# Kernel tuning notes

Hardware: AMD Instinct MI355X
Metric: run time of the kernel (lower is better)

Reference implementation:

```python
import jax, jax.numpy as jnp
import numpy as np

V, E, H, L = 32000, 512, 1024, 2
B, S, T = 32, 64, 64


def setup_inputs() -> dict:
    key = jax.random.key(0)
    ks = jax.random.split(key, 16)
    sd = 0.05
    p = lambda k, shape: (jax.random.normal(k, shape, jnp.float32) * sd)
    z = lambda shape: jnp.zeros(shape, jnp.float32)
    return {
        "tgt_batch": jax.random.randint(ks[0], (B, S), 0, V),
        "enc_h": p(ks[1], (L, B, H)),
        "enc_c": p(ks[2], (L, B, H)),
        "enc_outputs": p(ks[3], (T, B, H)),
        "emb": p(ks[4], (V, E)),
        "W_ih0": p(ks[5], (4 * H, E + H)),
        "W_hh0": p(ks[6], (4 * H, H)),
        "b_ih0": z((4 * H,)),
        "b_hh0": z((4 * H,)),
        "W_ih1": p(ks[7], (4 * H, H)),
        "W_hh1": p(ks[8], (4 * H, H)),
        "b_ih1": z((4 * H,)),
        "b_hh1": z((4 * H,)),
        "Wa": p(ks[9], (H, 2 * H)),
        "ba": z((H,)),
        "va": p(ks[10], (H,)),
        "Wc": p(ks[11], (H, 2 * H)),
        "bc": z((H,)),
        "Wo": p(ks[12], (V, H)),
        "bo": z((V,)),
        "teacher_forcing": 1,
    }


def _lstm_cell(x, h, c, Wih, Whh, bih, bhh):
    # PyTorch gate order: i, f, g, o
    g = x @ Wih.T + bih + h @ Whh.T + bhh
    i, f, gg, o = jnp.split(g, 4, axis=1)
    c2 = jax.nn.sigmoid(f) * c + jax.nn.sigmoid(i) * jnp.tanh(gg)
    return jax.nn.sigmoid(o) * jnp.tanh(c2), c2


def reference(tgt_batch, enc_h, enc_c, enc_outputs, emb,
              W_ih0, W_hh0, b_ih0, b_hh0, W_ih1, W_hh1, b_ih1, b_hh1,
              Wa, ba, va, Wc, bc, Wo, bo, teacher_forcing):
    # teacher_forcing == 1 -> always feed the gold previous word (matches
    # the torch loop, whose sampling branch is never taken at tf=1.0).
    tgt = tgt_batch.T  # [S, B], seq-first

    def step(carry, x_t):
        h, c, attn_h = carry  # h,c: [L,B,H]; attn_h: [B,H]
        x = jnp.concatenate([emb[x_t], attn_h], axis=1)  # [B, E+H]
        h0, c0 = _lstm_cell(x, h[0], c[0], W_ih0, W_hh0, b_ih0, b_hh0)
        h1, c1 = _lstm_cell(h0, h[1], c[1], W_ih1, W_hh1, b_ih1, b_hh1)
        # additive ('concat') attention over encoder states, query = top h
        hid = jnp.broadcast_to(h1[None], enc_outputs.shape)  # [T,B,H]
        energy = jnp.tanh(jnp.concatenate([hid, enc_outputs], axis=-1) @ Wa.T + ba)
        scores = jnp.einsum('tbh,h->bt', energy, va)  # [B,T]
        weights = jax.nn.softmax(scores, axis=1)
        context = jnp.einsum('bt,tbh->bh', weights, enc_outputs)  # [B,H]
        attn_h2 = jnp.tanh(jnp.concatenate([h1, context], axis=1) @ Wc.T + bc)
        logp = jax.nn.log_softmax(attn_h2 @ Wo.T + bo, axis=1)  # [B,V]
        return (jnp.stack([h0, h1]), jnp.stack([c0, c1]), attn_h2), logp

    init = (enc_h, enc_c, jnp.zeros((tgt.shape[1], H), enc_h.dtype))
    _, dec_outputs = jax.lax.scan(step, init, tgt[:-1])  # [S-1, B, V]
    dec_output_words = jnp.argmax(dec_outputs, axis=-1).astype(jnp.int32)
    return dec_outputs, dec_output_words
```

## Files before the change

kernel.cpp:

```cpp
#include <hip/hip_runtime.h>
#include <math.h>

#define VOCAB 32000
#define EMBD  512
#define HID   1024
#define BATCH 32
#define SEQ   64
#define TENC  64
#define NSTEP 63
#define G4    4096

typedef __attribute__((ext_vector_type(8))) short short8;
typedef __attribute__((ext_vector_type(4))) float f32x4;
typedef __attribute__((ext_vector_type(4))) unsigned short us4;

__device__ __forceinline__ float4 ld4(const float* p) {
  return *reinterpret_cast<const float4*>(p);
}
__device__ __forceinline__ unsigned short f2bf(float x) {
  unsigned u = __float_as_uint(x);
  return (unsigned short)((u + 0x7fffu + ((u >> 16) & 1u)) >> 16);
}
__device__ __forceinline__ float bf2f(unsigned short h) {
  return __uint_as_float(((unsigned)h) << 16);
}

template<class FA, class FW>
__device__ __forceinline__ void g32x4(int team, int ttid, FA fa, FW fw, int KT,
                                      float* tiles, float* res) {
  float* At = tiles + team * 2176;
  float* Wt = At + 1088;
  const int lr = ttid >> 3, lc = (ttid & 7) << 2;
  const int tn = ttid & 15, tm = ttid >> 4;
  float a00=0.f, a01=0.f, a10=0.f, a11=0.f;
  float4 av = fa(lc);
  float4 wv = fw(lc);
  for (int k0 = 0; k0 < KT; k0 += 32) {
    float4 avn, wvn;
    if (k0 + 32 < KT) { avn = fa(k0 + 32 + lc); wvn = fw(k0 + 32 + lc); }
    __syncthreads();
    At[(lc+0)*34+lr]=av.x; At[(lc+1)*34+lr]=av.y; At[(lc+2)*34+lr]=av.z; At[(lc+3)*34+lr]=av.w;
    Wt[(lc+0)*34+lr]=wv.x; Wt[(lc+1)*34+lr]=wv.y; Wt[(lc+2)*34+lr]=wv.z; Wt[(lc+3)*34+lr]=wv.w;
    __syncthreads();
    #pragma unroll
    for (int kk = 0; kk < 32; ++kk) {
      const float2 a = *reinterpret_cast<const float2*>(&At[kk*34 + tm*2]);
      const float2 w = *reinterpret_cast<const float2*>(&Wt[kk*34 + tn*2]);
      a00 += a.x*w.x; a01 += a.x*w.y; a10 += a.y*w.x; a11 += a.y*w.y;
    }
    av = avn; wv = wvn;
  }
  float* r = res + team * 1056;
  r[(tm*2  )*33 + tn*2  ] = a00;
  r[(tm*2  )*33 + tn*2+1] = a01;
  r[(tm*2+1)*33 + tn*2  ] = a10;
  r[(tm*2+1)*33 + tn*2+1] = a11;
}

__device__ __forceinline__ void whh_block(const float* h, const float* W, float* C,
                                          int nt, int ldc, float* tiles, float* res) {
  const int tid = threadIdx.x, team = tid >> 8, ttid = tid & 255;
  const int lr = ttid >> 3;
  const int kb = team * 256;
  const float* Ap = h + lr*HID + kb;
  const float* Wp = W + (size_t)(nt*32 + lr)*HID + kb;
  g32x4(team, ttid, [=](int k){ return ld4(Ap + k); },
        [=](int k){ return ld4(Wp + k); }, 256, tiles, res);
  __syncthreads();
  const int b = tid >> 5, cc = tid & 31;
  const float v = res[b*33+cc] + res[1056 + b*33+cc]
                + res[2112 + b*33+cc] + res[3168 + b*33+cc];
  C[(size_t)b*ldc + nt*32 + cc] = v;
}

struct GC {
  const int* tgt; const float* emb;
  const float* A;
  const float* W;
  const float* gembt; const float* PgH; const float* bsum;
  float* h; float* c; int t;
};

template<int LAYER, int HOIST>
__device__ __forceinline__ void gcell_block(const GC& P, int nt, float* tiles, float* res) {
  const int tid = threadIdx.x, team = tid >> 8, ttid = tid & 255;
  const int lr = ttid >> 3;
  const int wrow = (lr >> 3)*1024 + nt*8 + (lr & 7);
  if (LAYER == 0) {
    if (HOIST) {
      const int kb = team * 256;
      const float* Ap = P.A + lr*HID + kb;
      const float* Wp = P.W + (size_t)wrow*(EMBD+HID) + EMBD + kb;
      g32x4(team, ttid, [=](int k){ return ld4(Ap + k); },
            [=](int k){ return ld4(Wp + k); }, 256, tiles, res);
    } else {
      const int kb = team * 384;
      const float* Wp = P.W + (size_t)wrow*(EMBD+HID) + kb;
      const int tok = P.tgt[lr*SEQ + P.t];
      const float* Ep = P.emb + (size_t)tok*EMBD;
      const float* Ap = P.A + lr*HID;
      g32x4(team, ttid,
            [=](int k){ const int kg = kb + k;
                        return (kg < EMBD) ? ld4(Ep + kg) : ld4(Ap + kg - EMBD); },
            [=](int k){ return ld4(Wp + k); }, 384, tiles, res);
    }
  } else {
    const int kb = team * 256;
    const float* Ap = P.A + lr*HID + kb;
    const float* Wp = P.W + (size_t)wrow*HID + kb;
    g32x4(team, ttid, [=](int k){ return ld4(Ap + k); },
          [=](int k){ return ld4(Wp + k); }, 256, tiles, res);
  }
  __syncthreads();
  if (tid < 256) {
    const int b = tid >> 3, j = tid & 7;
    const int n = nt*8 + j;
    float g4v[4];
    #pragma unroll
    for (int g = 0; g < 4; ++g) {
      const int gcol = g*1024 + n;
      const int r = g*8 + j;
      float s = P.bsum[gcol] + P.PgH[(size_t)b*G4 + gcol]
              + res[b*33+r] + res[1056 + b*33+r] + res[2112 + b*33+r] + res[3168 + b*33+r];
      if (LAYER == 0 && HOIST) s += P.gembt[(size_t)b*G4 + gcol];
      g4v[g] = s;
    }
    const float si = 1.f/(1.f+expf(-g4v[0]));
    const float sf = 1.f/(1.f+expf(-g4v[1]));
    const float so = 1.f/(1.f+expf(-g4v[3]));
    const int i = b*HID + n;
    const float cn = sf*P.c[i] + si*tanhf(g4v[2]);
    P.c[i] = cn;
    P.h[i] = so*tanhf(cn);
  }
}

template<int HOIST>
__global__ __launch_bounds__(1024) void l1_k(GC P) {
  __shared__ float tiles[4*2176];
  __shared__ float res[4*1056];
  gcell_block<0,HOIST>(P, blockIdx.x, tiles, res);
}

struct L2P { GC gc; const float* h0; const float* Whh0; float* PgH0; };

__global__ __launch_bounds__(1024) void l2_k(L2P P) {
  __shared__ float tiles[4*2176];
  __shared__ float res[4*1056];
  const int bid = blockIdx.x;
  if (bid < 128) gcell_block<1,0>(P.gc, bid, tiles, res);
  else           whh_block(P.h0, P.Whh0, P.PgH0, bid - 128, G4, tiles, res);
}

struct L3P { const float* h1; const float* Wa; const float* Wc; float* Pq; };

__global__ __launch_bounds__(1024) void l3_k(L3P P) {
  __shared__ float tiles[4*2176];
  __shared__ float res[4*1056];
  const int nt = blockIdx.x;
  const int tid = threadIdx.x, team = tid >> 8, ttid = tid & 255;
  const int lr = ttid >> 3;
  const int kb = team * 256;
  const int row = nt*32 + lr;
  const float* Ap = P.h1 + lr*HID + kb;
  const float* Wp = ((row < HID) ? (P.Wa + (size_t)row*(2*HID))
                                 : (P.Wc + (size_t)(row - HID)*(2*HID))) + kb;
  g32x4(team, ttid, [=](int k){ return ld4(Ap + k); },
        [=](int k){ return ld4(Wp + k); }, 256, tiles, res);
  __syncthreads();
  const int b = tid >> 5, cc = tid & 31;
  const float v = res[b*33+cc] + res[1056 + b*33+cc]
                + res[2112 + b*33+cc] + res[3168 + b*33+cc];
  P.Pq[(size_t)b*2048 + nt*32 + cc] = v;
}

struct L4P {
  const float* Pq; const float* PreAC; const float* va; const float* bc;
  const float* h1; const float* Whh1;
  float* AHt; float* PgH1;
};

__global__ __launch_bounds__(1024) void l4_k(L4P P) {
  __shared__ float tiles[4*2176];
  __shared__ float res[4*1056];
  const int bid = blockIdx.x;
  const int tid = threadIdx.x;
  if (bid < 32) {
    const int b = bid;
    float* QS  = tiles;
    float* sw  = tiles + 1024;
    float* W64 = tiles + 1088;
    QS[tid] = P.Pq[(size_t)b*2048 + tid];
    __syncthreads();
    const int lane = tid & 63, wid = tid >> 6;
    float vreg[16];
    #pragma unroll
    for (int i2 = 0; i2 < 16; ++i2) vreg[i2] = P.va[lane + 64*i2];
    #pragma unroll
    for (int j = 0; j < 4; ++j) {
      const int te = wid*4 + j;
      const float* pr = P.PreAC + ((size_t)te*BATCH + b)*2048;
      float s = 0.f;
      #pragma unroll
      for (int i2 = 0; i2 < 16; ++i2) {
        const int idx = lane + 64*i2;
        s += vreg[i2] * tanhf(QS[idx] + pr[idx]);
      }
      #pragma unroll
      for (int off = 32; off; off >>= 1) s += __shfl_xor(s, off);
      if (lane == 0) sw[te] = s;
    }
    __syncthreads();
    if (tid < TENC) {
      const float v = sw[tid];
      float mx = v;
      #pragma unroll
      for (int off = 32; off; off >>= 1) mx = fmaxf(mx, __shfl_xor(mx, off));
      const float e = expf(v - mx);
      float sum = e;
      #pragma unroll
      for (int off = 32; off; off >>= 1) sum += __shfl_xor(sum, off);
      W64[tid] = e / sum;
    }
    __syncthreads();
    const int hh = tid;
    float acc = 0.f;
    #pragma unroll 8
    for (int te = 0; te < TENC; ++te)
      acc += W64[te] * P.PreAC[((size_t)te*BATCH + b)*2048 + HID + hh];
    const float hc = P.Pq[(size_t)b*2048 + HID + hh] + P.bc[hh];
    P.AHt[(size_t)b*HID + hh] = tanhf(acc + hc);
  } else {
    whh_block(P.h1, P.Whh1, P.PgH1, bid - 32, G4, tiles, res);
  }
}

struct WIP {
  const float* h0; const float* h1; const float* Whh0; const float* Whh1;
  float* PgH0; float* PgH1;
};

__global__ __launch_bounds__(1024) void whhinit_k(WIP P) {
  __shared__ float tiles[4*2176];
  __shared__ float res[4*1056];
  const int bid = blockIdx.x;
  if (bid < 128) whh_block(P.h0, P.Whh0, P.PgH0, bid, G4, tiles, res);
  else           whh_block(P.h1, P.Whh1, P.PgH1, bid - 128, G4, tiles, res);
}

struct WGP {
  const float* A; const float* W; const float* W2; const float* bias;
  const int* tgt; const float* emb;
  float* C; int ldc;
};

template<int WM>
__device__ __forceinline__ float4 ldWL(const WGP& P, int r, int k) {
  if (WM == 0) return ld4(P.W + (size_t)r * 1024 + k);
  if (WM == 2) return ld4(P.W + (size_t)r * (EMBD + HID) + k);
  if (r < HID) return ld4(P.W  + (size_t)r * (2*HID) + HID + k);
  return ld4(P.W2 + (size_t)(r - HID) * (2*HID) + HID + k);
}

template<int WM>
__device__ __forceinline__ float4 ldAL(const WGP& P, int row, int k) {
  if (WM == 2) {
    const int tok = P.tgt[(row & 31) * SEQ + (row >> 5)];
    return ld4(P.emb + (size_t)tok * EMBD + k);
  }
  return ld4(P.A + (size_t)row * 1024 + k);
}

template<int WM>
__global__ __launch_bounds__(256, 2) void gemmL(WGP P) {
  constexpr int KK = (WM == 2) ? 512 : 1024;
  __shared__ float At[32*36];
  __shared__ float Wt[32*260];
  const int tid = threadIdx.x;
  const int m0 = blockIdx.x * 32;
  const int n0 = blockIdx.y * 256;
  const int lr = tid >> 3, lc = (tid & 7) << 2;
  const int tn = tid & 31, tm = tid >> 5;
  float acc[4][8];
  #pragma unroll
  for (int i = 0; i < 4; ++i)
    #pragma unroll
    for (int x = 0; x < 8; ++x) acc[i][x] = 0.f;

  float4 av = ldAL<WM>(P, m0 + lr, lc);
  float4 wv[8];
  #pragma unroll
  for (int it = 0; it < 8; ++it) wv[it] = ldWL<WM>(P, n0 + lr + it*32, lc);

  for (int k0 = 0; k0 < KK; k0 += 32) {
    float4 avn, wvn[8];
    if (k0 + 32 < KK) {
      avn = ldAL<WM>(P, m0 + lr, k0 + 32 + lc);
      #pragma unroll
      for (int it = 0; it < 8; ++it) wvn[it] = ldWL<WM>(P, n0 + lr + it*32, k0 + 32 + lc);
    }
    __syncthreads();
    At[(lc+0)*36+lr]=av.x; At[(lc+1)*36+lr]=av.y; At[(lc+2)*36+lr]=av.z; At[(lc+3)*36+lr]=av.w;
    #pragma unroll
    for (int it = 0; it < 8; ++it) {
      const int r = lr + it*32;
      Wt[(lc+0)*260+r]=wv[it].x; Wt[(lc+1)*260+r]=wv[it].y;
      Wt[(lc+2)*260+r]=wv[it].z; Wt[(lc+3)*260+r]=wv[it].w;
    }
    __syncthreads();
    #pragma unroll
    for (int kk = 0; kk < 32; ++kk) {
      const float4 a  = *reinterpret_cast<const float4*>(&At[kk*36 + tm*4]);
      const float4 w0 = *reinterpret_cast<const float4*>(&Wt[kk*260 + tn*8]);
      const float4 w1 = *reinterpret_cast<const float4*>(&Wt[kk*260 + tn*8 + 4]);
      #pragma unroll
      for (int i = 0; i < 4; ++i) {
        const float ai = (&a.x)[i];
        acc[i][0]+=ai*w0.x; acc[i][1]+=ai*w0.y; acc[i][2]+=ai*w0.z; acc[i][3]+=ai*w0.w;
        acc[i][4]+=ai*w1.x; acc[i][5]+=ai*w1.y; acc[i][6]+=ai*w1.z; acc[i][7]+=ai*w1.w;
      }
    }
    av = avn;
    #pragma unroll
    for (int it = 0; it < 8; ++it) wv[it] = wvn[it];
  }
  const int na = n0 + tn*8, ma = m0 + tm*4;
  float bb[8];
  #pragma unroll
  for (int x = 0; x < 8; ++x) {
    if (WM == 0)      bb[x] = P.bias[na+x];
    else if (WM == 1) bb[x] = (na + x < HID) ? P.bias[na+x] : 0.f;
    else              bb[x] = 0.f;
  }
  #pragma unroll
  for (int i = 0; i < 4; ++i)
    #pragma unroll
    for (int x = 0; x < 8; ++x)
      P.C[(size_t)(ma+i)*P.ldc + na + x] = acc[i][x] + bb[x];
}

__global__ __launch_bounds__(256) void cvt_k(const float* __restrict__ src,
                                             unsigned short* __restrict__ hi,
                                             unsigned short* __restrict__ lo, int n) {
  int i = (blockIdx.x*256 + threadIdx.x) * 4;
  const int stride = gridDim.x * 256 * 4;
  for (; i < n; i += stride) {
    const float4 v = ld4(src + i);
    us4 h, l;
    h.x = f2bf(v.x); l.x = f2bf(v.x - bf2f(h.x));
    h.y = f2bf(v.y); l.y = f2bf(v.y - bf2f(h.y));
    h.z = f2bf(v.z); l.z = f2bf(v.z - bf2f(h.z));
    h.w = f2bf(v.w); l.w = f2bf(v.w - bf2f(h.w));
    *reinterpret_cast<us4*>(hi + i) = h;
    *reinterpret_cast<us4*>(lo + i) = l;
  }
}

struct LM {
  const unsigned short* Ahi; const unsigned short* Alo;
  const unsigned short* Bhi; const unsigned short* Blo;
  const float* bo; float* out;
};

__global__ __launch_bounds__(256) void logits_mfma(LM P) {
  __shared__ unsigned short sA[2][4][64][8];
  __shared__ unsigned short sB[2][4][128][8];
  const int tid = threadIdx.x;
  const int m0 = blockIdx.x * 64;
  const int n0 = blockIdx.y * 128;
  const int w = tid >> 6, l = tid & 63;
  const int mb = (w & 1) * 32, nb = (w >> 1) * 64;
  f32x4 acc[2][4];
  #pragma unroll
  for (int mt = 0; mt < 2; ++mt)
    #pragma unroll
    for (int nt = 0; nt < 4; ++nt) acc[mt][nt] = 0.f;

  const int arow = tid >> 2, akg = tid & 3;
  const int brow = tid >> 1, bkg = (tid & 1) * 2;
  short8 pah, pal, pbh0, pbh1, pbl0, pbl1;
  {
    const size_t ao = (size_t)(m0 + arow)*HID + akg*8;
    const size_t bo0 = (size_t)(n0 + brow)*HID + bkg*8;
    pah  = *reinterpret_cast<const short8*>(P.Ahi + ao);
    pal  = *reinterpret_cast<const short8*>(P.Alo + ao);
    pbh0 = *reinterpret_cast<const short8*>(P.Bhi + bo0);
    pbh1 = *reinterpret_cast<const short8*>(P.Bhi + bo0 + 8);
    pbl0 = *reinterpret_cast<const short8*>(P.Blo + bo0);
    pbl1 = *reinterpret_cast<const short8*>(P.Blo + bo0 + 8);
  }
  for (int kc = 0; kc < 32; ++kc) {
    __syncthreads();
    *reinterpret_cast<short8*>(&sA[0][akg][arow][0]) = pah;
    *reinterpret_cast<short8*>(&sA[1][akg][arow][0]) = pal;
    *reinterpret_cast<short8*>(&sB[0][bkg  ][brow][0]) = pbh0;
    *reinterpret_cast<short8*>(&sB[0][bkg+1][brow][0]) = pbh1;
    *reinterpret_cast<short8*>(&sB[1][bkg  ][brow][0]) = pbl0;
    *reinterpret_cast<short8*>(&sB[1][bkg+1][brow][0]) = pbl1;
    __syncthreads();
    if (kc + 1 < 32) {
      const size_t ao = (size_t)(m0 + arow)*HID + (kc+1)*32 + akg*8;
      const size_t bo0 = (size_t)(n0 + brow)*HID + (kc+1)*32 + bkg*8;
      pah  = *reinterpret_cast<const short8*>(P.Ahi + ao);
      pal  = *reinterpret_cast<const short8*>(P.Alo + ao);
      pbh0 = *reinterpret_cast<const short8*>(P.Bhi + bo0);
      pbh1 = *reinterpret_cast<const short8*>(P.Bhi + bo0 + 8);
      pbl0 = *reinterpret_cast<const short8*>(P.Blo + bo0);
      pbl1 = *reinterpret_cast<const short8*>(P.Blo + bo0 + 8);
    }
    const int kg = l >> 4, rr = l & 15;
    short8 ah[2], al[2];
    #pragma unroll
    for (int mt = 0; mt < 2; ++mt) {
      ah[mt] = *reinterpret_cast<const short8*>(&sA[0][kg][mb + mt*16 + rr][0]);
      al[mt] = *reinterpret_cast<const short8*>(&sA[1][kg][mb + mt*16 + rr][0]);
    }
    #pragma unroll
    for (int nt = 0; nt < 4; ++nt) {
      const short8 bh = *reinterpret_cast<const short8*>(&sB[0][kg][nb + nt*16 + rr][0]);
      const short8 bl = *reinterpret_cast<const short8*>(&sB[1][kg][nb + nt*16 + rr][0]);
      #pragma unroll
      for (int mt = 0; mt < 2; ++mt) {
        acc[mt][nt] = __builtin_amdgcn_mfma_f32_16x16x32_bf16(ah[mt], bh, acc[mt][nt], 0, 0, 0);
        acc[mt][nt] = __builtin_amdgcn_mfma_f32_16x16x32_bf16(ah[mt], bl, acc[mt][nt], 0, 0, 0);
        acc[mt][nt] = __builtin_amdgcn_mfma_f32_16x16x32_bf16(al[mt], bh, acc[mt][nt], 0, 0, 0);
      }
    }
  }
  #pragma unroll
  for (int mt = 0; mt < 2; ++mt) {
    #pragma unroll
    for (int nt = 0; nt < 4; ++nt) {
      #pragma unroll
      for (int r = 0; r < 4; ++r) {
        const int row = m0 + mb + mt*16 + (l >> 4)*4 + r;
        const int col = n0 + nb + nt*16 + (l & 15);
        if (row < NSTEP*BATCH)
          P.out[(size_t)row*VOCAB + col] = acc[mt][nt][r] + P.bo[col];
      }
    }
  }
}

__global__ __launch_bounds__(256) void lsm_k(float* __restrict__ out,
                                             float* __restrict__ words) {
  const int b = blockIdx.x;
  const int t = blockIdx.y;
  float* row = out + ((size_t)t*BATCH + b)*VOCAB;
  const int tid = threadIdx.x;
  float m = -INFINITY; int mi = 0;
  for (int v = tid; v < VOCAB; v += 256) {
    const float x = row[v];
    if (x > m) { m = x; mi = v; }
  }
  __shared__ float sm[256]; __shared__ int si[256];
  sm[tid] = m; si[tid] = mi;
  __syncthreads();
  for (int s2 = 128; s2; s2 >>= 1) {
    if (tid < s2) {
      const float om = sm[tid+s2]; const int oi = si[tid+s2];
      if (om > sm[tid] || (om == sm[tid] && oi < si[tid])) { sm[tid]=om; si[tid]=oi; }
    }
    __syncthreads();
  }
  const float mx = sm[0]; const int amax = si[0];
  float s = 0.f;
  for (int v = tid; v < VOCAB; v += 256) s += expf(row[v]-mx);
  __shared__ float ss[256];
  ss[tid] = s; __syncthreads();
  for (int s2=128; s2; s2>>=1) { if (tid < s2) ss[tid] += ss[tid+s2]; __syncthreads(); }
  const float lse = logf(ss[0]) + mx;
  for (int v = tid; v < VOCAB; v += 256) row[v] = row[v] - lse;
  if (tid == 0) words[(size_t)t*BATCH + b] = (float)amax;
}

__global__ __launch_bounds__(256) void init_k(const float* __restrict__ enc_h,
                                              const float* __restrict__ enc_c,
                                              const float* __restrict__ bih0,
                                              const float* __restrict__ bhh0,
                                              const float* __restrict__ bih1,
                                              const float* __restrict__ bhh1,
                                              float* h0, float* h1, float* c0,
                                              float* c1, float* zbuf,
                                              float* bsum0, float* bsum1) {
  const int i = blockIdx.x*256 + threadIdx.x;
  if (i < BATCH*HID) {
    h0[i] = enc_h[i]; h1[i] = enc_h[BATCH*HID + i];
    c0[i] = enc_c[i]; c1[i] = enc_c[BATCH*HID + i];
    zbuf[i] = 0.f;
  }
  if (i < G4) {
    bsum0[i] = bih0[i] + bhh0[i];
    bsum1[i] = bih1[i] + bhh1[i];
  }
}

extern "C" void kernel_launch(void* const* d_in, const int* in_sizes, int n_in,
                              void* d_out, int out_size, void* d_ws, size_t ws_size,
                              hipStream_t stream) {
  const int*   tgt   = (const int*)d_in[0];
  const float* enc_h = (const float*)d_in[1];
  const float* enc_c = (const float*)d_in[2];
  const float* enc   = (const float*)d_in[3];
  const float* emb   = (const float*)d_in[4];
  const float* Wih0  = (const float*)d_in[5];
  const float* Whh0  = (const float*)d_in[6];
  const float* bih0  = (const float*)d_in[7];
  const float* bhh0  = (const float*)d_in[8];
  const float* Wih1  = (const float*)d_in[9];
  const float* Whh1  = (const float*)d_in[10];
  const float* bih1  = (const float*)d_in[11];
  const float* bhh1  = (const float*)d_in[12];
  const float* Wa    = (const float*)d_in[13];
  const float* ba    = (const float*)d_in[14];
  const float* va    = (const float*)d_in[15];
  const float* Wc    = (const float*)d_in[16];
  const float* bc    = (const float*)d_in[17];
  const float* Wo    = (const float*)d_in[18];
  const float* bo    = (const float*)d_in[19];

  float* ws = (float*)d_ws;
  float* AH = ws;
  float* pool = AH + (size_t)2048*1024;
  size_t off = 0;
  auto alloc = [&](size_t n) { float* p = pool + off; off += n; return p; };
  float* PreAC = alloc((size_t)2048*2048);
  float* Pq    = alloc((size_t)BATCH*2048);
  float* PgH0  = alloc((size_t)BATCH*G4);
  float* PgH1  = alloc((size_t)BATCH*G4);
  float* h0    = alloc(BATCH*HID);
  float* h1v   = alloc(BATCH*HID);
  float* c0    = alloc(BATCH*HID);
  float* c1v   = alloc(BATCH*HID);
  float* zbuf  = alloc(BATCH*HID);
  float* bsum0 = alloc(G4);
  float* bsum1 = alloc(G4);
  float* Gemb  = pool + off;
  const size_t loop_f = (size_t)(pool - ws) + off + (size_t)NSTEP*BATCH*G4;
  const bool hoist = ws_size >= loop_f * sizeof(float);

  const size_t nAH = (size_t)2048*1024, nWo = (size_t)VOCAB*1024;
  unsigned short* AHhi = (unsigned short*)pool;
  unsigned short* AHlo = AHhi + nAH;
  unsigned short* Wohi = AHlo + nAH;
  unsigned short* Wolo = Wohi + nWo;
  const bool mfma_ok =
      ws_size >= (size_t)2048*1024*sizeof(float) + (2*nAH + 2*nWo)*sizeof(unsigned short);

  float* out   = (float*)d_out;
  float* words = out + (size_t)NSTEP*BATCH*VOCAB;

  init_k<<<dim3(128), 256, 0, stream>>>(enc_h, enc_c, bih0, bhh0, bih1, bhh1,
                                        h0, h1v, c0, c1v, zbuf, bsum0, bsum1);

  {
    WGP p = {}; p.A = enc; p.W = Wa; p.W2 = Wc; p.bias = ba; p.C = PreAC; p.ldc = 2048;
    gemmL<1><<<dim3(64, 8), 256, 0, stream>>>(p);
  }
  if (hoist) {
    WGP p = {}; p.W = Wih0; p.tgt = tgt; p.emb = emb; p.C = Gemb; p.ldc = G4;
    gemmL<2><<<dim3(NSTEP*BATCH/32, G4/256), 256, 0, stream>>>(p);
  }
  {
    WIP p; p.h0 = h0; p.h1 = h1v; p.Whh0 = Whh0; p.Whh1 = Whh1;
    p.PgH0 = PgH0; p.PgH1 = PgH1;
    whhinit_k<<<dim3(256), 1024, 0, stream>>>(p);
  }

  for (int t = 0; t < NSTEP; ++t) {
    const float* ah_prev = t ? (AH + (size_t)(t-1)*BATCH*HID) : zbuf;
    {
      GC p = {}; p.tgt = tgt; p.emb = emb; p.t = t;
      p.A = ah_prev; p.W = Wih0;
      p.gembt = Gemb + (size_t)t*BATCH*G4;
      p.PgH = PgH0; p.bsum = bsum0; p.h = h0; p.c = c0;
      if (hoist) l1_k<1><<<dim3(128), 1024, 0, stream>>>(p);
      else       l1_k<0><<<dim3(128), 1024, 0, stream>>>(p);
    }
    {
      L2P p = {};
      p.gc.A = h0; p.gc.W = Wih1; p.gc.PgH = PgH1; p.gc.bsum = bsum1;
      p.gc.h = h1v; p.gc.c = c1v; p.gc.t = t;
      p.h0 = h0; p.Whh0 = Whh0; p.PgH0 = PgH0;
      l2_k<<<dim3(256), 1024, 0, stream>>>(p);
    }
    {
      L3P p; p.h1 = h1v; p.Wa = Wa; p.Wc = Wc; p.Pq = Pq;
      l3_k<<<dim3(64), 1024, 0, stream>>>(p);
    }
    {
      L4P p; p.Pq = Pq; p.PreAC = PreAC; p.va = va; p.bc = bc;
      p.h1 = h1v; p.Whh1 = Whh1;
      p.AHt = AH + (size_t)t*BATCH*HID; p.PgH1 = PgH1;
      l4_k<<<dim3(160), 1024, 0, stream>>>(p);
    }
  }

  if (mfma_ok) {
    cvt_k<<<dim3(4096), 256, 0, stream>>>(Wo, Wohi, Wolo, VOCAB*1024);
    cvt_k<<<dim3(2048), 256, 0, stream>>>(AH, AHhi, AHlo, NSTEP*BATCH*HID);
    LM p; p.Ahi = AHhi; p.Alo = AHlo; p.Bhi = Wohi; p.Blo = Wolo;
    p.bo = bo; p.out = out;
    logits_mfma<<<dim3(32, VOCAB/128), 256, 0, stream>>>(p);
  } else {
    WGP p = {}; p.A = AH; p.W = Wo; p.bias = bo; p.C = out; p.ldc = VOCAB;
    gemmL<0><<<dim3(NSTEP*BATCH/32, VOCAB/256), 256, 0, stream>>>(p);
  }
  lsm_k<<<dim3(BATCH, NSTEP), 256, 0, stream>>>(out, words);
}
```

Measured before the change: 7.072 ms.

## Move recurrent LSTM and attention projections to split-bf16 MFMA kernels

Replaces the per-step fp32 shared-memory GEMMs for both LSTM layers and the Wa/Wc query projection with MFMA kernels that use hi/lo bf16 splitting (three MFMAs per product) for near-fp32 accuracy. The weights are packed once into bf16 hi/lo with Wih and Whh concatenated along K, so each layer's gate GEMM covers both x and h in one pass. This removes the separate Whh kernels and the PgH buffers. Hidden states are double-buffered in bf16 hi/lo, and attention writes AH directly in split form, which drops the later conversion. The change adds weight-packing passes and a larger workspace, drops the fallbacks that checked workspace size, and runs 256-thread blocks with no LDS staging, relying on direct global loads.

Measured after the change: 5.914 ms. -16.4%, faster.

```diff
diff --git a/kernel.cpp b/kernel.cpp
--- a/kernel.cpp
+++ b/kernel.cpp
@@ -13,239 +13,251 @@
 typedef __attribute__((ext_vector_type(8))) short short8;
 typedef __attribute__((ext_vector_type(4))) float f32x4;
 typedef __attribute__((ext_vector_type(4))) unsigned short us4;
+typedef unsigned short u16;
 
 __device__ __forceinline__ float4 ld4(const float* p) {
   return *reinterpret_cast<const float4*>(p);
 }
-__device__ __forceinline__ unsigned short f2bf(float x) {
+__device__ __forceinline__ u16 f2bf(float x) {
   unsigned u = __float_as_uint(x);
-  return (unsigned short)((u + 0x7fffu + ((u >> 16) & 1u)) >> 16);
-}
-__device__ __forceinline__ float bf2f(unsigned short h) {
+  return (u16)((u + 0x7fffu + ((u >> 16) & 1u)) >> 16);
+}
+__device__ __forceinline__ float bf2f(u16 h) {
   return __uint_as_float(((unsigned)h) << 16);
 }
 
-template<class FA, class FW>
-__device__ __forceinline__ void g32x4(int team, int ttid, FA fa, FW fw, int KT,
-                                      float* tiles, float* res) {
-  float* At = tiles + team * 2176;
-  float* Wt = At + 1088;
-  const int lr = ttid >> 3, lc = (ttid & 7) << 2;
-  const int tn = ttid & 15, tm = ttid >> 4;
-  float a00=0.f, a01=0.f, a10=0.f, a11=0.f;
-  float4 av = fa(lc);
-  float4 wv = fw(lc);
-  for (int k0 = 0; k0 < KT; k0 += 32) {
-    float4 avn, wvn;
-    if (k0 + 32 < KT) { avn = fa(k0 + 32 + lc); wvn = fw(k0 + 32 + lc); }
-    __syncthreads();
-    At[(lc+0)*34+lr]=av.x; At[(lc+1)*34+lr]=av.y; At[(lc+2)*34+lr]=av.z; At[(lc+3)*34+lr]=av.w;
-    Wt[(lc+0)*34+lr]=wv.x; Wt[(lc+1)*34+lr]=wv.y; Wt[(lc+2)*34+lr]=wv.z; Wt[(lc+3)*34+lr]=wv.w;
-    __syncthreads();
-    #pragma unroll
-    for (int kk = 0; kk < 32; ++kk) {
-      const float2 a = *reinterpret_cast<const float2*>(&At[kk*34 + tm*2]);
-      const float2 w = *reinterpret_cast<const float2*>(&Wt[kk*34 + tn*2]);
-      a00 += a.x*w.x; a01 += a.x*w.y; a10 += a.y*w.x; a11 += a.y*w.y;
-    }
-    av = avn; wv = wvn;
-  }
-  float* r = res + team * 1056;
-  r[(tm*2  )*33 + tn*2  ] = a00;
-  r[(tm*2  )*33 + tn*2+1] = a01;
-  r[(tm*2+1)*33 + tn*2  ] = a10;
-  r[(tm*2+1)*33 + tn*2+1] = a11;
-}
-
-__device__ __forceinline__ void whh_block(const float* h, const float* W, float* C,
-                                          int nt, int ldc, float* tiles, float* res) {
-  const int tid = threadIdx.x, team = tid >> 8, ttid = tid & 255;
-  const int lr = ttid >> 3;
-  const int kb = team * 256;
-  const float* Ap = h + lr*HID + kb;
-  const float* Wp = W + (size_t)(nt*32 + lr)*HID + kb;
-  g32x4(team, ttid, [=](int k){ return ld4(Ap + k); },
-        [=](int k){ return ld4(Wp + k); }, 256, tiles, res);
+template<int MODE>
+__device__ __forceinline__ void mfma32(
+    const u16* __restrict__ Xahi, const u16* __restrict__ Xalo,
+    const u16* __restrict__ Xbhi, const u16* __restrict__ Xblo,
+    const u16* __restrict__ Whi,  const u16* __restrict__ Wlo,
+    int nt, float* res)
+{
+  const int tid = threadIdx.x;
+  const int w = tid >> 6, l = tid & 63;
+  const int c = l & 15, koct = l >> 4;
+  constexpr int K   = (MODE == 0) ? 2048 : 1024;
+  constexpr int WS  = (MODE == 0) ? 2048 : 1024;
+  constexpr int SPW = K / 32 / 4;
+  const int r0 = c, r1 = 16 + c;
+  const int wr0 = (MODE == 0) ? ((r0 >> 3)*1024 + nt*8 + (r0 & 7)) : (nt*32 + r0);
+  const int wr1 = (MODE == 0) ? ((r1 >> 3)*1024 + nt*8 + (r1 & 7)) : (nt*32 + r1);
+  const u16* bh0 = Whi + (size_t)wr0 * WS;
+  const u16* bh1 = Whi + (size_t)wr1 * WS;
+  const u16* bl0 = Wlo + (size_t)wr0 * WS;
+  const u16* bl1 = Wlo + (size_t)wr1 * WS;
+
+  auto ldA = [&](int m, int kg, int lo) -> short8 {
+    const u16* base;
+    if (MODE == 0 && kg >= 1024) base = lo ? Xblo : Xbhi;
+    else                         base = lo ? Xalo : Xahi;
+    const int b = m*16 + c;
+    return *reinterpret_cast<const short8*>(base + b*1024 + (kg & 1023));
+  };
+
+  f32x4 acc[2][2];
+  #pragma unroll
+  for (int m = 0; m < 2; ++m)
+    #pragma unroll
+    for (int n = 0; n < 2; ++n) acc[m][n] = (f32x4){0.f,0.f,0.f,0.f};
+
+  const int s0 = w * SPW;
+  short8 Ah[2], Al[2], Bh[2], Bl[2];
+  {
+    const int kg = s0*32 + koct*8;
+    Ah[0]=ldA(0,kg,0); Ah[1]=ldA(1,kg,0); Al[0]=ldA(0,kg,1); Al[1]=ldA(1,kg,1);
+    Bh[0]=*reinterpret_cast<const short8*>(bh0+kg);
+    Bh[1]=*reinterpret_cast<const short8*>(bh1+kg);
+    Bl[0]=*reinterpret_cast<const short8*>(bl0+kg);
+    Bl[1]=*reinterpret_cast<const short8*>(bl1+kg);
+  }
+  for (int s = s0; s < s0 + SPW; ++s) {
+    short8 nAh[2], nAl[2], nBh[2], nBl[2];
+    if (s + 1 < s0 + SPW) {
+      const int kg = (s+1)*32 + koct*8;
+      nAh[0]=ldA(0,kg,0); nAh[1]=ldA(1,kg,0); nAl[0]=ldA(0,kg,1); nAl[1]=ldA(1,kg,1);
+      nBh[0]=*reinterpret_cast<const short8*>(bh0+kg);
+      nBh[1]=*reinterpret_cast<const short8*>(bh1+kg);
+      nBl[0]=*reinterpret_cast<const short8*>(bl0+kg);
+      nBl[1]=*reinterpret_cast<const short8*>(bl1+kg);
+    }
+    #pragma unroll
+    for (int n = 0; n < 2; ++n)
+      #pragma unroll
+      for (int m = 0; m < 2; ++m) {
+        acc[m][n] = __builtin_amdgcn_mfma_f32_16x16x32_bf16(Ah[m], Bh[n], acc[m][n], 0, 0, 0);
+        acc[m][n] = __builtin_amdgcn_mfma_f32_16x16x32_bf16(Ah[m], Bl[n], acc[m][n], 0, 0, 0);
+        acc[m][n] = __builtin_amdgcn_mfma_f32_16x16x32_bf16(Al[m], Bh[n], acc[m][n], 0, 0, 0);
+      }
+    #pragma unroll
+    for (int i = 0; i < 2; ++i) { Ah[i]=nAh[i]; Al[i]=nAl[i]; Bh[i]=nBh[i]; Bl[i]=nBl[i]; }
+  }
+  #pragma unroll
+  for (int m = 0; m < 2; ++m)
+    #pragma unroll
+    for (int n = 0; n < 2; ++n)
+      #pragma unroll
+      for (int r = 0; r < 4; ++r) {
+        const int b = m*16 + koct*4 + r;
+        const int rr = n*16 + c;
+        res[w*1056 + b*33 + rr] = acc[m][n][r];
+      }
+}
+
+struct GKM {
+  const u16 *Xahi, *Xalo, *Xbhi, *Xblo;
+  const u16 *Whi, *Wlo;
+  const float* bsum; const float* gembt;
+  float* c; u16 *hhi; u16 *hlo;
+};
+
+template<int HASGEMB>
+__global__ __launch_bounds__(256) void gates_mfma_k(GKM P) {
+  __shared__ float res[4*1056];
+  mfma32<0>(P.Xahi, P.Xalo, P.Xbhi, P.Xblo, P.Whi, P.Wlo, blockIdx.x, res);
   __syncthreads();
-  const int b = tid >> 5, cc = tid & 31;
-  const float v = res[b*33+cc] + res[1056 + b*33+cc]
-                + res[2112 + b*33+cc] + res[3168 + b*33+cc];
-  C[(size_t)b*ldc + nt*32 + cc] = v;
-}
-
-struct GC {
-  const int* tgt; const float* emb;
-  const float* A;
-  const float* W;
-  const float* gembt; const float* PgH; const float* bsum;
-  float* h; float* c; int t;
+  const int tid = threadIdx.x;
+  const int b = tid >> 3, j = tid & 7;
+  const int n = blockIdx.x*8 + j;
+  float g4[4];
+  #pragma unroll
+  for (int g = 0; g < 4; ++g) {
+    const int r = g*8 + j;
+    float s = P.bsum[g*1024 + n]
+            + res[b*33+r] + res[1056 + b*33+r] + res[2112 + b*33+r] + res[3168 + b*33+r];
+    if (HASGEMB) s += P.gembt[(size_t)b*G4 + g*1024 + n];
+    g4[g] = s;
+  }
+  const float si = 1.f/(1.f+expf(-g4[0]));
+  const float sf = 1.f/(1.f+expf(-g4[1]));
+  const float so = 1.f/(1.f+expf(-g4[3]));
+  const int i = b*HID + n;
+  const float cn = sf*P.c[i] + si*tanhf(g4[2]);
+  P.c[i] = cn;
+  const float h = so*tanhf(cn);
+  const u16 hh = f2bf(h);
+  P.hhi[i] = hh;
+  P.hlo[i] = f2bf(h - bf2f(hh));
+}
+
+struct PKM {
+  const u16 *Xhi, *Xlo; const u16 *Whi, *Wlo; float* Pq;
 };
 
-template<int LAYER, int HOIST>
-__device__ __forceinline__ void gcell_block(const GC& P, int nt, float* tiles, float* res) {
-  const int tid = threadIdx.x, team = tid >> 8, ttid = tid & 255;
-  const int lr = ttid >> 3;
-  const int wrow = (lr >> 3)*1024 + nt*8 + (lr & 7);
-  if (LAYER == 0) {
-    if (HOIST) {
-      const int kb = team * 256;
-      const float* Ap = P.A + lr*HID + kb;
-      const float* Wp = P.W + (size_t)wrow*(EMBD+HID) + EMBD + kb;
-      g32x4(team, ttid, [=](int k){ return ld4(Ap + k); },
-            [=](int k){ return ld4(Wp + k); }, 256, tiles, res);
-    } else {
-      const int kb = team * 384;
-      const float* Wp = P.W + (size_t)wrow*(EMBD+HID) + kb;
-      const int tok = P.tgt[lr*SEQ + P.t];
-      const float* Ep = P.emb + (size_t)tok*EMBD;
-      const float* Ap = P.A + lr*HID;
-      g32x4(team, ttid,
-            [=](int k){ const int kg = kb + k;
-                        return (kg < EMBD) ? ld4(Ep + kg) : ld4(Ap + kg - EMBD); },
-            [=](int k){ return ld4(Wp + k); }, 384, tiles, res);
-    }
-  } else {
-    const int kb = team * 256;
-    const float* Ap = P.A + lr*HID + kb;
-    const float* Wp = P.W + (size_t)wrow*HID + kb;
-    g32x4(team, ttid, [=](int k){ return ld4(Ap + k); },
-          [=](int k){ return ld4(Wp + k); }, 256, tiles, res);
-  }
+__global__ __launch_bounds__(256) void proj_mfma_k(PKM P) {
+  __shared__ float res[4*1056];
+  mfma32<1>(P.Xhi, P.Xlo, nullptr, nullptr, P.Whi, P.Wlo, blockIdx.x, res);
   __syncthreads();
-  if (tid < 256) {
-    const int b = tid >> 3, j = tid & 7;
-    const int n = nt*8 + j;
-    float g4v[4];
-    #pragma unroll
-    for (int g = 0; g < 4; ++g) {
-      const int gcol = g*1024 + n;
-      const int r = g*8 + j;
-      float s = P.bsum[gcol] + P.PgH[(size_t)b*G4 + gcol]
-              + res[b*33+r] + res[1056 + b*33+r] + res[2112 + b*33+r] + res[3168 + b*33+r];
-      if (LAYER == 0 && HOIST) s += P.gembt[(size_t)b*G4 + gcol];
-      g4v[g] = s;
-    }
-    const float si = 1.f/(1.f+expf(-g4v[0]));
-    const float sf = 1.f/(1.f+expf(-g4v[1]));
-    const float so = 1.f/(1.f+expf(-g4v[3]));
-    const int i = b*HID + n;
-    const float cn = sf*P.c[i] + si*tanhf(g4v[2]);
-    P.c[i] = cn;
-    P.h[i] = so*tanhf(cn);
-  }
-}
-
-template<int HOIST>
-__global__ __launch_bounds__(1024) void l1_k(GC P) {
-  __shared__ float tiles[4*2176];
-  __shared__ float res[4*1056];
-  gcell_block<0,HOIST>(P, blockIdx.x, tiles, res);
-}
-
-struct L2P { GC gc; const float* h0; const float* Whh0; float* PgH0; };
-
-__global__ __launch_bounds__(1024) void l2_k(L2P P) {
-  __shared__ float tiles[4*2176];
-  __shared__ float res[4*1056];
-  const int bid = blockIdx.x;
-  if (bid < 128) gcell_block<1,0>(P.gc, bid, tiles, res);
-  else           whh_block(P.h0, P.Whh0, P.PgH0, bid - 128, G4, tiles, res);
-}
-
-struct L3P { const float* h1; const float* Wa; const float* Wc; float* Pq; };
-
-__global__ __launch_bounds__(1024) void l3_k(L3P P) {
-  __shared__ float tiles[4*2176];
-  __shared__ float res[4*1056];
-  const int nt = blockIdx.x;
-  const int tid = threadIdx.x, team = tid >> 8, ttid = tid & 255;
-  const int lr = ttid >> 3;
-  const int kb = team * 256;
-  const int row = nt*32 + lr;
-  const float* Ap = P.h1 + lr*HID + kb;
-  const float* Wp = ((row < HID) ? (P.Wa + (size_t)row*(2*HID))
-                                 : (P.Wc + (size_t)(row - HID)*(2*HID))) + kb;
-  g32x4(team, ttid, [=](int k){ return ld4(Ap + k); },
-        [=](int k){ return ld4(Wp + k); }, 256, tiles, res);
+  const int tid = threadIdx.x;
+  #pragma unroll
+  for (int q = 0; q < 4; ++q) {
+    const int o = q*256 + tid;
+    const int b = o >> 5, r = o & 31;
+    const float s = res[b*33+r] + res[1056 + b*33+r]
+                  + res[2112 + b*33+r] + res[3168 + b*33+r];
+    P.Pq[(size_t)b*2048 + blockIdx.x*32 + r] = s;
+  }
+}
+
+struct AKM {
+  const float* Pq; const float* PreAC; const float* va; const float* bc;
+  u16* AHthi; u16* AHtlo;
+};
+
+__global__ __launch_bounds__(1024) void attn_k(AKM P) {
+  __shared__ float QS[HID];
+  __shared__ float sw[TENC];
+  __shared__ float W64[TENC];
+  const int b = blockIdx.x;
+  const int tid = threadIdx.x;
+  QS[tid] = P.Pq[(size_t)b*2048 + tid];
   __syncthreads();
-  const int b = tid >> 5, cc = tid & 31;
-  const float v = res[b*33+cc] + res[1056 + b*33+cc]
-                + res[2112 + b*33+cc] + res[3168 + b*33+cc];
-  P.Pq[(size_t)b*2048 + nt*32 + cc] = v;
-}
-
-struct L4P {
-  const float* Pq; const float* PreAC; const float* va; const float* bc;
-  const float* h1; const float* Whh1;
-  float* AHt; float* PgH1;
-};
-
-__global__ __launch_bounds__(1024) void l4_k(L4P P) {
-  __shared__ float tiles[4*2176];
-  __shared__ float res[4*1056];
-  const int bid = blockIdx.x;
-  const int tid = threadIdx.x;
-  if (bid < 32) {
-    const int b = bid;
-    float* QS  = tiles;
-    float* sw  = tiles + 1024;
-    float* W64 = tiles + 1088;
-    QS[tid] = P.Pq[(size_t)b*2048 + tid];
-    __syncthreads();
-    const int lane = tid & 63, wid = tid >> 6;
-    float vreg[16];
-    #pragma unroll
-    for (int i2 = 0; i2 < 16; ++i2) vreg[i2] = P.va[lane + 64*i2];
-    #pragma unroll
-    for (int j = 0; j < 4; ++j) {
-      const int te = wid*4 + j;
-      const float* pr = P.PreAC + ((size_t)te*BATCH + b)*2048;
-      float s = 0.f;
-      #pragma unroll
-      for (int i2 = 0; i2 < 16; ++i2) {
-        const int idx = lane + 64*i2;
-        s += vreg[i2] * tanhf(QS[idx] + pr[idx]);
-      }
-      #pragma unroll
-      for (int off = 32; off; off >>= 1) s += __shfl_xor(s, off);
-      if (lane == 0) sw[te] = s;
-    }
-    __syncthreads();
-    if (tid < TENC) {
-      const float v = sw[tid];
-      float mx = v;
-      #pragma unroll
-      for (int off = 32; off; off >>= 1) mx = fmaxf(mx, __shfl_xor(mx, off));
-      const float e = expf(v - mx);
-      float sum = e;
-      #pragma unroll
-      for (int off = 32; off; off >>= 1) sum += __shfl_xor(sum, off);
-      W64[tid] = e / sum;
-    }
-    __syncthreads();
-    const int hh = tid;
-    float acc = 0.f;
-    #pragma unroll 8
-    for (int te = 0; te < TENC; ++te)
-      acc += W64[te] * P.PreAC[((size_t)te*BATCH + b)*2048 + HID + hh];
-    const float hc = P.Pq[(size_t)b*2048 + HID + hh] + P.bc[hh];
-    P.AHt[(size_t)b*HID + hh] = tanhf(acc + hc);
-  } else {
-    whh_block(P.h1, P.Whh1, P.PgH1, bid - 32, G4, tiles, res);
-  }
-}
-
-struct WIP {
-  const float* h0; const float* h1; const float* Whh0; const float* Whh1;
-  float* PgH0; float* PgH1;
-};
-
-__global__ __launch_bounds__(1024) void whhinit_k(WIP P) {
-  __shared__ float tiles[4*2176];
-  __shared__ float res[4*1056];
-  const int bid = blockIdx.x;
-  if (bid < 128) whh_block(P.h0, P.Whh0, P.PgH0, bid, G4, tiles, res);
-  else           whh_block(P.h1, P.Whh1, P.PgH1, bid - 128, G4, tiles, res);
+  const int lane = tid & 63, wid = tid >> 6;
+  float vreg[16];
+  #pragma unroll
+  for (int i2 = 0; i2 < 16; ++i2) vreg[i2] = P.va[lane + 64*i2];
+  #pragma unroll
+  for (int j = 0; j < 4; ++j) {
+    const int te = wid*4 + j;
+    const float* pr = P.PreAC + ((size_t)te*BATCH + b)*2048;
+    float s = 0.f;
+    #pragma unroll
+    for (int i2 = 0; i2 < 16; ++i2) {
+      const int idx = lane + 64*i2;
+      s += vreg[i2] * tanhf(QS[idx] + pr[idx]);
+    }
+    #pragma unroll
+    for (int off = 32; off; off >>= 1) s += __shfl_xor(s, off);
+    if (lane == 0) sw[te] = s;
+  }
+  __syncthreads();
+  if (tid < TENC) {
+    const float v = sw[tid];
+    float mx = v;
+    #pragma unroll
+    for (int off = 32; off; off >>= 1) mx = fmaxf(mx, __shfl_xor(mx, off));
+    const float e = expf(v - mx);
+    float sum = e;
+    #pragma unroll
+    for (int off = 32; off; off >>= 1) sum += __shfl_xor(sum, off);
+    W64[tid] = e / sum;
+  }
+  __syncthreads();
+  const int hh = tid;
+  float acc = 0.f;
+  #pragma unroll 8
+  for (int te = 0; te < TENC; ++te)
+    acc += W64[te] * P.PreAC[((size_t)te*BATCH + b)*2048 + HID + hh];
+  const float hc = P.Pq[(size_t)b*2048 + HID + hh] + P.bc[hh];
+  const float ah = tanhf(acc + hc);
+  const u16 ahh = f2bf(ah);
+  P.AHthi[(size_t)b*HID + hh] = ahh;
+  P.AHtlo[(size_t)b*HID + hh] = f2bf(ah - bf2f(ahh));
+}
+
+template<int MODE>
+__global__ __launch_bounds__(256) void pack_k(const float* __restrict__ A,
+                                              const float* __restrict__ B,
+                                              u16* __restrict__ hi, u16* __restrict__ lo) {
+  constexpr int ROWS = (MODE == 2) ? 2048 : 4096;
+  constexpr int K    = (MODE == 2) ? 1024 : 2048;
+  const size_t total = (size_t)ROWS * (K/4);
+  for (size_t i = (size_t)blockIdx.x*256 + threadIdx.x; i < total;
+       i += (size_t)gridDim.x*256) {
+    const int row = (int)(i / (K/4));
+    const int k = (int)(i % (K/4)) * 4;
+    float4 v;
+    if (MODE == 0) v = (k < 1024) ? ld4(A + (size_t)row*1536 + 512 + k)
+                                  : ld4(B + (size_t)row*1024 + (k - 1024));
+    else if (MODE == 1) v = (k < 1024) ? ld4(A + (size_t)row*1024 + k)
+                                       : ld4(B + (size_t)row*1024 + (k - 1024));
+    else v = (row < 1024) ? ld4(A + (size_t)row*2048 + k)
+                          : ld4(B + (size_t)(row - 1024)*2048 + k);
+    us4 h, l;
+    h.x = f2bf(v.x); l.x = f2bf(v.x - bf2f(h.x));
+    h.y = f2bf(v.y); l.y = f2bf(v.y - bf2f(h.y));
+    h.z = f2bf(v.z); l.z = f2bf(v.z - bf2f(h.z));
+    h.w = f2bf(v.w); l.w = f2bf(v.w - bf2f(h.w));
+    *reinterpret_cast<us4*>(hi + i*4) = h;
+    *reinterpret_cast<us4*>(lo + i*4) = l;
+  }
+}
+
+__global__ __launch_bounds__(256) void cvt_k(const float* __restrict__ src,
+                                             u16* __restrict__ hi,
+                                             u16* __restrict__ lo, int n) {
+  int i = (blockIdx.x*256 + threadIdx.x) * 4;
+  const int stride = gridDim.x * 256 * 4;
+  for (; i < n; i += stride) {
+    const float4 v = ld4(src + i);
+    us4 h, l;
+    h.x = f2bf(v.x); l.x = f2bf(v.x - bf2f(h.x));
+    h.y = f2bf(v.y); l.y = f2bf(v.y - bf2f(h.y));
+    h.z = f2bf(v.z); l.z = f2bf(v.z - bf2f(h.z));
+    h.w = f2bf(v.w); l.w = f2bf(v.w - bf2f(h.w));
+    *reinterpret_cast<us4*>(hi + i) = h;
+    *reinterpret_cast<us4*>(lo + i) = l;
+  }
 }
 
 struct WGP {
@@ -256,7 +268,6 @@
 
 template<int WM>
 __device__ __forceinline__ float4 ldWL(const WGP& P, int r, int k) {
-  if (WM == 0) return ld4(P.W + (size_t)r * 1024 + k);
   if (WM == 2) return ld4(P.W + (size_t)r * (EMBD + HID) + k);
   if (r < HID) return ld4(P.W  + (size_t)r * (2*HID) + HID + k);
   return ld4(P.W2 + (size_t)(r - HID) * (2*HID) + HID + k);
@@ -328,9 +339,8 @@
   float bb[8];
   #pragma unroll
   for (int x = 0; x < 8; ++x) {
-    if (WM == 0)      bb[x] = P.bias[na+x];
-    else if (WM == 1) bb[x] = (na + x < HID) ? P.bias[na+x] : 0.f;
-    else              bb[x] = 0.f;
+    if (WM == 1) bb[x] = (na + x < HID) ? P.bias[na+x] : 0.f;
+    else         bb[x] = 0.f;
   }
   #pragma unroll
   for (int i = 0; i < 4; ++i)
@@ -339,32 +349,15 @@
       P.C[(size_t)(ma+i)*P.ldc + na + x] = acc[i][x] + bb[x];
 }
 
-__global__ __launch_bounds__(256) void cvt_k(const float* __restrict__ src,
-                                             unsigned short* __restrict__ hi,
-                                             unsigned short* __restrict__ lo, int n) {
-  int i = (blockIdx.x*256 + threadIdx.x) * 4;
-  const int stride = gridDim.x * 256 * 4;
-  for (; i < n; i += stride) {
-    const float4 v = ld4(src + i);
-    us4 h, l;
-    h.x = f2bf(v.x); l.x = f2bf(v.x - bf2f(h.x));
-    h.y = f2bf(v.y); l.y = f2bf(v.y - bf2f(h.y));
-    h.z = f2bf(v.z); l.z = f2bf(v.z - bf2f(h.z));
-    h.w = f2bf(v.w); l.w = f2bf(v.w - bf2f(h.w));
-    *reinterpret_cast<us4*>(hi + i) = h;
-    *reinterpret_cast<us4*>(lo + i) = l;
-  }
-}
-
 struct LM {
-  const unsigned short* Ahi; const unsigned short* Alo;
-  const unsigned short* Bhi; const unsigned short* Blo;
+  const u16* Ahi; const u16* Alo;
+  const u16* Bhi; const u16* Blo;
   const float* bo; float* out;
 };
 
 __global__ __launch_bounds__(256) void logits_mfma(LM P) {
-  __shared__ unsigned short sA[2][4][64][8];
-  __shared__ unsigned short sB[2][4][128][8];
+  __shared__ u16 sA[2][4][64][8];
+  __shared__ u16 sB[2][4][128][8];
   const int tid = threadIdx.x;
   const int m0 = blockIdx.x * 64;
   const int n0 = blockIdx.y * 128;
@@ -374,7 +367,7 @@
   #pragma unroll
   for (int mt = 0; mt < 2; ++mt)
     #pragma unroll
-    for (int nt = 0; nt < 4; ++nt) acc[mt][nt] = 0.f;
+    for (int nt = 0; nt < 4; ++nt) acc[mt][nt] = (f32x4){0.f,0.f,0.f,0.f};
 
   const int arow = tid >> 2, akg = tid & 3;
   const int brow = tid >> 1, bkg = (tid & 1) * 2;
@@ -480,14 +473,20 @@
                                               const float* __restrict__ bhh0,
                                               const float* __restrict__ bih1,
                                               const float* __restrict__ bhh1,
-                                              float* h0, float* h1, float* c0,
-                                              float* c1, float* zbuf,
+                                              float* c0, float* c1,
+                                              u16* h0hi, u16* h0lo, u16* h1hi, u16* h1lo,
+                                              u16* zahhi, u16* zahlo,
                                               float* bsum0, float* bsum1) {
   const int i = blockIdx.x*256 + threadIdx.x;
   if (i < BATCH*HID) {
-    h0[i] = enc_h[i]; h1[i] = enc_h[BATCH*HID + i];
     c0[i] = enc_c[i]; c1[i] = enc_c[BATCH*HID + i];
-    zbuf[i] = 0.f;
+    const float v0 = enc_h[i];
+    const u16 h0 = f2bf(v0);
+    h0hi[i] = h0; h0lo[i] = f2bf(v0 - bf2f(h0));
+    const float v1 = enc_h[BATCH*HID + i];
+    const u16 h1 = f2bf(v1);
+    h1hi[i] = h1; h1lo[i] = f2bf(v1 - bf2f(h1));
+    zahhi[i] = 0; zahlo[i] = 0;
   }
   if (i < G4) {
     bsum0[i] = bih0[i] + bhh0[i];
@@ -519,92 +518,100 @@
   const float* Wo    = (const float*)d_in[18];
   const float* bo    = (const float*)d_in[19];
 
-  float* ws = (float*)d_ws;
-  float* AH = ws;
-  float* pool = AH + (size_t)2048*1024;
-  size_t off = 0;
-  auto alloc = [&](size_t n) { float* p = pool + off; off += n; return p; };
-  float* PreAC = alloc((size_t)2048*2048);
-  float* Pq    = alloc((size_t)BATCH*2048);
-  float* PgH0  = alloc((size_t)BATCH*G4);
-  float* PgH1  = alloc((size_t)BATCH*G4);
-  float* h0    = alloc(BATCH*HID);
-  float* h1v   = alloc(BATCH*HID);
-  float* c0    = alloc(BATCH*HID);
-  float* c1v   = alloc(BATCH*HID);
-  float* zbuf  = alloc(BATCH*HID);
-  float* bsum0 = alloc(G4);
-  float* bsum1 = alloc(G4);
-  float* Gemb  = pool + off;
-  const size_t loop_f = (size_t)(pool - ws) + off + (size_t)NSTEP*BATCH*G4;
-  const bool hoist = ws_size >= loop_f * sizeof(float);
-
-  const size_t nAH = (size_t)2048*1024, nWo = (size_t)VOCAB*1024;
-  unsigned short* AHhi = (unsigned short*)pool;
-  unsigned short* AHlo = AHhi + nAH;
-  unsigned short* Wohi = AHlo + nAH;
-  unsigned short* Wolo = Wohi + nWo;
-  const bool mfma_ok =
-      ws_size >= (size_t)2048*1024*sizeof(float) + (2*nAH + 2*nWo)*sizeof(unsigned short);
+  u16* AHhi = (u16*)d_ws;
+  u16* AHlo = AHhi + (size_t)2048*1024;
+  float* pool = (float*)(AHlo + (size_t)2048*1024);
+
+  float* PreAC = pool;
+  float* Gemb  = PreAC + (size_t)2048*2048;
+  float* Pq    = Gemb  + (size_t)NSTEP*BATCH*G4;
+  float* c0    = Pq    + (size_t)BATCH*2048;
+  float* c1v   = c0    + BATCH*HID;
+  float* bsum0 = c1v   + BATCH*HID;
+  float* bsum1 = bsum0 + G4;
+  u16* W0hi = (u16*)(bsum1 + G4);
+  u16* W0lo = W0hi + (size_t)4096*2048;
+  u16* W1hi = W0lo + (size_t)4096*2048;
+  u16* W1lo = W1hi + (size_t)4096*2048;
+  u16* WAhi = W1lo + (size_t)4096*2048;
+  u16* WAlo = WAhi + (size_t)2048*1024;
+  u16* h0Ahi = WAlo + (size_t)2048*1024;
+  u16* h0Alo = h0Ahi + BATCH*HID;
+  u16* h0Bhi = h0Alo + BATCH*HID;
+  u16* h0Blo = h0Bhi + BATCH*HID;
+  u16* h1Ahi = h0Blo + BATCH*HID;
+  u16* h1Alo = h1Ahi + BATCH*HID;
+  u16* h1Bhi = h1Alo + BATCH*HID;
+  u16* h1Blo = h1Bhi + BATCH*HID;
+  u16* zahhi = h1Blo + BATCH*HID;
+  u16* zahlo = zahhi + BATCH*HID;
+  u16* Wohi = (u16*)pool;
+  u16* Wolo = Wohi + (size_t)VOCAB*1024;
 
   float* out   = (float*)d_out;
   float* words = out + (size_t)NSTEP*BATCH*VOCAB;
 
   init_k<<<dim3(128), 256, 0, stream>>>(enc_h, enc_c, bih0, bhh0, bih1, bhh1,
-                                        h0, h1v, c0, c1v, zbuf, bsum0, bsum1);
+                                        c0, c1v, h0Ahi, h0Alo, h1Ahi, h1Alo,
+                                        zahhi, zahlo, bsum0, bsum1);
 
   {
     WGP p = {}; p.A = enc; p.W = Wa; p.W2 = Wc; p.bias = ba; p.C = PreAC; p.ldc = 2048;
     gemmL<1><<<dim3(64, 8), 256, 0, stream>>>(p);
   }
-  if (hoist) {
+  {
     WGP p = {}; p.W = Wih0; p.tgt = tgt; p.emb = emb; p.C = Gemb; p.ldc = G4;
     gemmL<2><<<dim3(NSTEP*BATCH/32, G4/256), 256, 0, stream>>>(p);
   }
+  pack_k<0><<<dim3(1024), 256, 0, stream>>>(Wih0, Whh0, W0hi, W0lo);
+  pack_k<1><<<dim3(1024), 256, 0, stream>>>(Wih1, Whh1, W1hi, W1lo);
+  pack_k<2><<<dim3(512), 256, 0, stream>>>(Wa, Wc, WAhi, WAlo);
+
+  for (int t = 0; t < NSTEP; ++t) {
+    const u16* ahphi = t ? (AHhi + (size_t)(t-1)*BATCH*HID) : zahhi;
+    const u16* ahplo = t ? (AHlo + (size_t)(t-1)*BATCH*HID) : zahlo;
+    const u16* h0phi = (t & 1) ? h0Bhi : h0Ahi;
+    const u16* h0plo = (t & 1) ? h0Blo : h0Alo;
+    u16* h0chi = (t & 1) ? h0Ahi : h0Bhi;
+    u16* h0clo = (t & 1) ? h0Alo : h0Blo;
+    const u16* h1phi = (t & 1) ? h1Bhi : h1Ahi;
+    const u16* h1plo = (t & 1) ? h1Blo : h1Alo;
+    u16* h1chi = (t & 1) ? h1Ahi : h1Bhi;
+    u16* h1clo = (t & 1) ? h1Alo : h1Blo;
+
+    {
+      GKM p = {};
+      p.Xahi = ahphi; p.Xalo = ahplo; p.Xbhi = h0phi; p.Xblo = h0plo;
+      p.Whi = W0hi; p.Wlo = W0lo;
+      p.bsum = bsum0; p.gembt = Gemb + (size_t)t*BATCH*G4;
+      p.c = c0; p.hhi = h0chi; p.hlo = h0clo;
+      gates_mfma_k<1><<<dim3(128), 256, 0, stream>>>(p);
+    }
+    {
+      GKM p = {};
+      p.Xahi = h0chi; p.Xalo = h0clo; p.Xbhi = h1phi; p.Xblo = h1plo;
+      p.Whi = W1hi; p.Wlo = W1lo;
+      p.bsum = bsum1; p.gembt = nullptr;
+      p.c = c1v; p.hhi = h1chi; p.hlo = h1clo;
+      gates_mfma_k<0><<<dim3(128), 256, 0, stream>>>(p);
+    }
+    {
+      PKM p; p.Xhi = h1chi; p.Xlo = h1clo; p.Whi = WAhi; p.Wlo = WAlo; p.Pq = Pq;
+      proj_mfma_k<<<dim3(64), 256, 0, stream>>>(p);
+    }
+    {
+      AKM p; p.Pq = Pq; p.PreAC = PreAC; p.va = va; p.bc = bc;
+      p.AHthi = AHhi + (size_t)t*BATCH*HID;
+      p.AHtlo = AHlo + (size_t)t*BATCH*HID;
+      attn_k<<<dim3(BATCH), 1024, 0, stream>>>(p);
+    }
+  }
+
+  cvt_k<<<dim3(4096), 256, 0, stream>>>(Wo, Wohi, Wolo, VOCAB*1024);
   {
-    WIP p; p.h0 = h0; p.h1 = h1v; p.Whh0 = Whh0; p.Whh1 = Whh1;
-    p.PgH0 = PgH0; p.PgH1 = PgH1;
-    whhinit_k<<<dim3(256), 1024, 0, stream>>>(p);
-  }
-
-  for (int t = 0; t < NSTEP; ++t) {
-    const float* ah_prev = t ? (AH + (size_t)(t-1)*BATCH*HID) : zbuf;
-    {
-      GC p = {}; p.tgt = tgt; p.emb = emb; p.t = t;
-      p.A = ah_prev; p.W = Wih0;
-      p.gembt = Gemb + (size_t)t*BATCH*G4;
-      p.PgH = PgH0; p.bsum = bsum0; p.h = h0; p.c = c0;
-      if (hoist) l1_k<1><<<dim3(128), 1024, 0, stream>>>(p);
-      else       l1_k<0><<<dim3(128), 1024, 0, stream>>>(p);
-    }
-    {
-      L2P p = {};
-      p.gc.A = h0; p.gc.W = Wih1; p.gc.PgH = PgH1; p.gc.bsum = bsum1;
-      p.gc.h = h1v; p.gc.c = c1v; p.gc.t = t;
-      p.h0 = h0; p.Whh0 = Whh0; p.PgH0 = PgH0;
-      l2_k<<<dim3(256), 1024, 0, stream>>>(p);
-    }
-    {
-      L3P p; p.h1 = h1v; p.Wa = Wa; p.Wc = Wc; p.Pq = Pq;
-      l3_k<<<dim3(64), 1024, 0, stream>>>(p);
-    }
-    {
-      L4P p; p.Pq = Pq; p.PreAC = PreAC; p.va = va; p.bc = bc;
-      p.h1 = h1v; p.Whh1 = Whh1;
-      p.AHt = AH + (size_t)t*BATCH*HID; p.PgH1 = PgH1;
-      l4_k<<<dim3(160), 1024, 0, stream>>>(p);
-    }
-  }
-
-  if (mfma_ok) {
-    cvt_k<<<dim3(4096), 256, 0, stream>>>(Wo, Wohi, Wolo, VOCAB*1024);
-    cvt_k<<<dim3(2048), 256, 0, stream>>>(AH, AHhi, AHlo, NSTEP*BATCH*HID);
     LM p; p.Ahi = AHhi; p.Alo = AHlo; p.Bhi = Wohi; p.Blo = Wolo;
     p.bo = bo; p.out = out;
     logits_mfma<<<dim3(32, VOCAB/128), 256, 0, stream>>>(p);
-  } else {
-    WGP p = {}; p.A = AH; p.W = Wo; p.bias = bo; p.C = out; p.ldc = VOCAB;
-    gemmL<0><<<dim3(NSTEP*BATCH/32, VOCAB/256), 256, 0, stream>>>(p);
   }
   lsm_k<<<dim3(BATCH, NSTEP), 256, 0, stream>>>(out, words);
 }
```
